# Optimization experiments

Hardware: AMD Instinct MI355X
Metric: run time of the kernel (lower is better)

The kernel has to match this reference:

```python
import jax, jax.numpy as jnp
import numpy as np
import math

NH = 16  # n_head
HS = 64  # head_size = n_embd // n_head


def setup_inputs() -> dict:
    key = jax.random.key(0)
    ks = jax.random.split(key, 7)
    B, T, C, QL, KVL = 2, 2048, 1024, 128, 128
    s = lambda k, shape, fan_in: jax.random.normal(k, shape, jnp.float32) / np.sqrt(fan_in)
    return {
        "x": jax.random.normal(ks[0], (B, T, C), jnp.float32),
        "W_dq": s(ks[1], (QL, C), C),
        "W_uq": s(ks[2], (C, QL), QL),
        "W_dkv": s(ks[3], (KVL, C), C),
        "W_uk": s(ks[4], (C, KVL), KVL),
        "W_uv": s(ks[5], (C, KVL), KVL),
        "W_o": s(ks[6], (C, C), C),
    }


def reference(x, W_dq, W_uq, W_dkv, W_uk, W_uv, W_o):
    B, T, C = x.shape
    kvl = W_dkv.shape[0]
    # absorbed matrices (training branch)
    k_eff = (W_dq.T @ W_uq.T @ W_uk).reshape(NH, HS, kvl)            # (nh, hs, kvl)
    v_eff = (W_uv.T @ W_o.T).reshape(kvl, NH, HS).transpose(1, 0, 2)  # (nh, kvl, hs)
    # latent kv cache
    c_kv = x @ W_dkv.T                                                # (B, T, kvl)
    # query path
    q = (x @ W_dq.T @ W_uq.T).reshape(B, T, NH, HS).transpose(0, 2, 1, 3)  # (B, nh, T, hs)
    # scores: q @ k_eff @ c_kv^T
    ql = jnp.einsum('bhtd,hdl->bhtl', q, k_eff)                       # (B, nh, T, kvl)
    scores = jnp.einsum('bhtl,bsl->bhts', ql, c_kv) / math.sqrt(HS)   # (B, nh, T, T)
    # causal mask
    mask = jnp.tril(jnp.ones((T, T), dtype=bool))
    scores = jnp.where(mask[None, None], scores, -jnp.inf)
    attn = jax.nn.softmax(scores, axis=-1)
    # output: attn @ c_kv @ v_eff
    ctx = jnp.einsum('bhts,bsl->bhtl', attn, c_kv)                    # (B, nh, T, kvl)
    y = jnp.einsum('bhtl,hld->bhtd', ctx, v_eff)                      # (B, nh, T, hs)
    y = y.transpose(0, 2, 1, 3).reshape(B, T, C)
    return y, c_kv
```

## Files before the change

### kernel.cpp

```cpp
#include <hip/hip_runtime.h>
#include <hip/hip_bf16.h>

typedef __hip_bfloat16 bf16;
typedef __attribute__((ext_vector_type(8))) short short8;
typedef __attribute__((ext_vector_type(4))) float f32x4;

#define NHD 16
#define HSD 64
#define KVLD 128
#define QLD 128
#define CD 1024
#define BD 2
#define TD 2048

__device__ __forceinline__ short8 ld8(const bf16* p) { return *(const short8*)p; }
__device__ __forceinline__ void st8(bf16* p, short8 v) { *(short8*)p = v; }

__device__ __forceinline__ void st4(bf16* p, float4 a) {
    union { short4 s; bf16 h[4]; } u;
    u.h[0] = __float2bfloat16(a.x); u.h[1] = __float2bfloat16(a.y);
    u.h[2] = __float2bfloat16(a.z); u.h[3] = __float2bfloat16(a.w);
    *(short4*)p = u.s;
}
__device__ __forceinline__ void st4f(bf16* p, f32x4 a) {
    union { short4 s; bf16 h[4]; } u;
    u.h[0] = __float2bfloat16(a[0]); u.h[1] = __float2bfloat16(a[1]);
    u.h[2] = __float2bfloat16(a[2]); u.h[3] = __float2bfloat16(a[3]);
    *(short4*)p = u.s;
}

__global__ __launch_bounds__(256) void k_pre(const float* __restrict__ wuq,
                                             const float* __restrict__ wuk,
                                             const float* __restrict__ wdq,
                                             const float* __restrict__ wdkv,
                                             const float* __restrict__ wuv,
                                             const float* __restrict__ wo,
                                             float* __restrict__ m1p,
                                             float* __restrict__ G,
                                             bf16* __restrict__ wqkv_bf,
                                             bf16* __restrict__ veffT_bf) {
    __shared__ __align__(16) char arena[49152];
    const int b = blockIdx.x;
    const int tid = threadIdx.x;
    if (b < 128) {
        const int part = b >> 4, ig = b & 15;
        const int i = ig * 8 + (tid >> 5);
        const int j4 = (tid & 31) << 2;
        const float* wq = wuq + (size_t)part * 128 * QLD;
        const float* wk = wuk + (size_t)part * 128 * KVLD;
        float4 acc = make_float4(0.f, 0.f, 0.f, 0.f);
        for (int c0 = 0; c0 < 128; c0 += 8) {
            float a[8]; float4 kv[8];
#pragma unroll
            for (int u = 0; u < 8; ++u) {
                a[u] = wq[(c0 + u) * QLD + i];
                kv[u] = *(const float4*)(wk + (c0 + u) * KVLD + j4);
            }
#pragma unroll
            for (int u = 0; u < 8; ++u) {
                acc.x = fmaf(a[u], kv[u].x, acc.x);
                acc.y = fmaf(a[u], kv[u].y, acc.y);
                acc.z = fmaf(a[u], kv[u].z, acc.z);
                acc.w = fmaf(a[u], kv[u].w, acc.w);
            }
        }
        *(float4*)(m1p + (size_t)part * 16384 + (size_t)i * 128 + j4) = acc;
    } else if (b < 256) {
        const int b1 = b - 128;
        const int h = b1 >> 3, p8 = b1 & 7;
        const int p = p8 * 16 + (tid >> 4);
        const int i8 = (tid & 15) << 3;
        float acc[8];
#pragma unroll
        for (int t = 0; t < 8; ++t) acc[t] = 0.f;
        const float* wdqp = wdq + (size_t)p * CD + h * 64;
        const float* wuqh = wuq + (size_t)(h * 64) * QLD + i8;
        for (int d0 = 0; d0 < 64; d0 += 8) {
            float a[8]; float4 b0[8], b1v[8];
#pragma unroll
            for (int u = 0; u < 8; ++u) {
                a[u] = wdqp[d0 + u];
                b0[u] = *(const float4*)(wuqh + (d0 + u) * QLD);
                b1v[u] = *(const float4*)(wuqh + (d0 + u) * QLD + 4);
            }
#pragma unroll
            for (int u = 0; u < 8; ++u) {
                acc[0] = fmaf(a[u], b0[u].x, acc[0]);  acc[1] = fmaf(a[u], b0[u].y, acc[1]);
                acc[2] = fmaf(a[u], b0[u].z, acc[2]);  acc[3] = fmaf(a[u], b0[u].w, acc[3]);
                acc[4] = fmaf(a[u], b1v[u].x, acc[4]); acc[5] = fmaf(a[u], b1v[u].y, acc[5]);
                acc[6] = fmaf(a[u], b1v[u].z, acc[6]); acc[7] = fmaf(a[u], b1v[u].w, acc[7]);
            }
        }
        float* dst = G + (size_t)h * 16384 + (size_t)p * 128 + i8;
        *(float4*)dst = make_float4(acc[0], acc[1], acc[2], acc[3]);
        *(float4*)(dst + 4) = make_float4(acc[4], acc[5], acc[6], acc[7]);
    } else if (b < 320) {
        const int r = (b - 256) * 4 + (tid >> 6);
        const int lane = tid & 63;
        const float* src = (r < 128) ? (wdq + (size_t)r * CD) : (wdkv + (size_t)(r - 128) * CD);
        float4 f[4];
#pragma unroll
        for (int k = 0; k < 4; ++k) f[k] = ((const float4*)src)[lane + k * 64];
#pragma unroll
        for (int k = 0; k < 4; ++k)
            st4(wqkv_bf + (size_t)r * CD + (lane + k * 64) * 4, f[k]);
    } else {
        const int b3 = b - 320;
        const int cc0 = b3 * 4;
        float* woS = (float*)arena;
        float* wuvS = (float*)arena + 4096;
#pragma unroll
        for (int k = 0; k < 4; ++k)
            ((float4*)woS)[tid + k * 256] = ((const float4*)(wo + (size_t)cc0 * CD))[tid + k * 256];

        const int r = tid >> 6;
        const int lh = tid & 63;
        float4 pf[8];
#pragma unroll
        for (int t = 0; t < 8; ++t)
            pf[t] = ((const float4*)wuv)[t * 256 + tid];

        float a0 = 0.f, a1 = 0.f;
        for (int ch = 0; ch < 16; ++ch) {
            __syncthreads();
#pragma unroll
            for (int t = 0; t < 8; ++t)
                ((float4*)wuvS)[t * 256 + tid] = pf[t];
            __syncthreads();
            if (ch < 15) {
#pragma unroll
                for (int t = 0; t < 8; ++t)
                    pf[t] = ((const float4*)wuv)[(ch + 1) * 2048 + t * 256 + tid];
            }
            const float* wr = woS + r * 1024 + ch * 64;
            const float2* vv = (const float2*)wuvS + lh;
            for (int cb = 0; cb < 64; cb += 8) {
                float wv[8]; float2 v[8];
#pragma unroll
                for (int u = 0; u < 8; ++u) {
                    wv[u] = wr[cb + u];
                    v[u] = vv[(cb + u) * 64];
                }
#pragma unroll
                for (int u = 0; u < 8; ++u) {
                    a0 = fmaf(wv[u], v[u].x, a0);
                    a1 = fmaf(wv[u], v[u].y, a1);
                }
            }
        }
        union { short2 s; bf16 h2[2]; } u;
        u.h2[0] = __float2bfloat16(a0);
        u.h2[1] = __float2bfloat16(a1);
        *(short2*)(veffT_bf + (size_t)(cc0 + r) * KVLD + lh * 2) = u.s;
    }
}

__global__ __launch_bounds__(256) void k_main(const float* __restrict__ x,
                                              const bf16* __restrict__ wqkv_bf,
                                              const float* __restrict__ m1p,
                                              const float* __restrict__ G,
                                              bf16* __restrict__ q1_bf,
                                              float* __restrict__ ckv_out,
                                              bf16* __restrict__ ckv_bf,
                                              bf16* __restrict__ ckvT_bf,
                                              bf16* __restrict__ Et_bf) {
    __shared__ __align__(16) char arena[39168];
    const int blk = blockIdx.x;
    const int tid = threadIdx.x;

    if (blk < 256) {
        const int m0 = blk * 16;
        const int w = tid >> 6, lane = tid & 63, m16 = lane & 15, g = lane >> 4;
        bf16* As = (bf16*)arena;
        bf16* Bs = (bf16*)(arena + 2304);

        const int arow = tid >> 4, akc = (tid & 15) << 2;
        const float* axp = x + (size_t)(m0 + arow) * CD + akc;
        int brow[8], bkc[8];
#pragma unroll
        for (int kk = 0; kk < 8; ++kk) {
            int v = tid + kk * 256;
            brow[kk] = v >> 3; bkc[kk] = (v & 7) << 3;
        }

        float4 pA = *(const float4*)(axp);
        short8 pB[8];
#pragma unroll
        for (int kk = 0; kk < 8; ++kk)
            pB[kk] = ld8(wqkv_bf + (size_t)brow[kk] * CD + bkc[kk]);

        f32x4 acc[4];
#pragma unroll
        for (int nb = 0; nb < 4; ++nb) acc[nb] = (f32x4){0.f, 0.f, 0.f, 0.f};

        for (int k0 = 0; k0 < CD; k0 += 64) {
            __syncthreads();
            st4(As + arow * 72 + akc, pA);
#pragma unroll
            for (int kk = 0; kk < 8; ++kk)
                st8(Bs + brow[kk] * 72 + bkc[kk], pB[kk]);
            __syncthreads();
            if (k0 + 64 < CD) {
                pA = *(const float4*)(axp + k0 + 64);
#pragma unroll
                for (int kk = 0; kk < 8; ++kk)
                    pB[kk] = ld8(wqkv_bf + (size_t)brow[kk] * CD + k0 + 64 + bkc[kk]);
            }
            short8 aF[2];
#pragma unroll
            for (int kf = 0; kf < 2; ++kf)
                aF[kf] = ld8(As + m16 * 72 + kf * 32 + g * 8);
#pragma unroll
            for (int nb = 0; nb < 4; ++nb)
#pragma unroll
                for (int kf = 0; kf < 2; ++kf) {
                    short8 bF = ld8(Bs + (w * 64 + nb * 16 + m16) * 72 + kf * 32 + g * 8);
                    acc[nb] = __builtin_amdgcn_mfma_f32_16x16x32_bf16(aF[kf], bF, acc[nb], 0, 0, 0);
                }
        }

        const int bb = m0 >> 11;
        const int tl0 = (m0 & 2047) + g * 4;
#pragma unroll
        for (int nb = 0; nb < 4; ++nb) {
            int col = w * 64 + nb * 16 + m16;
            if (col < 128) {
#pragma unroll
                for (int r = 0; r < 4; ++r)
                    q1_bf[(size_t)(m0 + g * 4 + r) * QLD + col] = __float2bfloat16(acc[nb][r]);
            } else {
                int l = col - 128;
                union { short4 s; bf16 h[4]; } pk;
#pragma unroll
                for (int r = 0; r < 4; ++r) {
                    int t = m0 + g * 4 + r;
                    float v = acc[nb][r];
                    ckv_out[(size_t)t * KVLD + l] = v;
                    bf16 hv = __float2bfloat16(v);
                    ckv_bf[(size_t)t * KVLD + l] = hv;
                    pk.h[r] = hv;
                }
                *(short4*)(ckvT_bf + ((size_t)bb * KVLD + l) * TD + tl0) = pk.s;
            }
        }
    } else {
        const int b2 = blk - 256;
        const int h = b2 >> 4, lb = b2 & 15;
        float* m1s = (float*)arena;
        for (int v = tid; v < 1024; v += 256) {
            int p = v >> 3, lq = v & 7;
            float t0[8];
#pragma unroll
            for (int part = 0; part < 8; ++part)
                t0[part] = m1p[(size_t)part * 16384 + (size_t)p * 128 + lb * 8 + lq];
            float s0 = 0.f;
#pragma unroll
            for (int part = 0; part < 8; ++part) s0 += t0[part];
            m1s[v] = s0;
        }
        __syncthreads();
        const int lq = tid >> 5, i4 = (tid & 31) << 2;
        const float* Gh = G + (size_t)h * 16384;
        float4 acc = make_float4(0.f, 0.f, 0.f, 0.f);
        for (int p0 = 0; p0 < 128; p0 += 8) {
            float4 g[8]; float a[8];
#pragma unroll
            for (int u = 0; u < 8; ++u) {
                g[u] = *(const float4*)(Gh + (p0 + u) * 128 + i4);
                a[u] = m1s[(p0 + u) * 8 + lq];
            }
#pragma unroll
            for (int u = 0; u < 8; ++u) {
                acc.x = fmaf(a[u], g[u].x, acc.x);
                acc.y = fmaf(a[u], g[u].y, acc.y);
                acc.z = fmaf(a[u], g[u].z, acc.z);
                acc.w = fmaf(a[u], g[u].w, acc.w);
            }
        }
        const float sc = 0.1803368801f;
        const int l = lb * 8 + lq;
        st4(Et_bf + ((size_t)h * 128 + l) * 128 + i4,
            make_float4(sc * acc.x, sc * acc.y, sc * acc.z, sc * acc.w));
    }
}

__global__ __launch_bounds__(512, 4) void k_flash(const bf16* __restrict__ Q1_bf,
                                                  const bf16* __restrict__ Et_bf,
                                                  const bf16* __restrict__ ckv_bf,
                                                  const bf16* __restrict__ ckvT_bf,
                                                  const bf16* __restrict__ veffT_bf,
                                                  float* __restrict__ yout) {
    const int h = blockIdx.x & 15;
    const int b = blockIdx.x >> 4;
    const int qlo = blockIdx.y;
    const int qhi = 31 - qlo;
    const int tid = threadIdx.x;
    const int w = tid >> 6;
    const int ws = w >> 2;
    const int wq = w & 3;
    const int lane = tid & 63;
    const int m16 = lane & 15;
    const int g = lane >> 4;
    const int myqt = ws ? qlo : qhi;
    const int row0 = myqt * 64;

    __shared__ __align__(16) short smem_raw[27136];
    bf16* smem = (bf16*)smem_raw;
    bf16* kvN = smem;
    bf16* kvT = smem + 8704;
    bf16* pS  = smem + 17920 + w * 1152;
    bf16* bufLo = kvT;
    bf16* vT = smem + 17920;

    {
        const bf16* q1hi = Q1_bf + ((size_t)(b * TD + qhi * 64)) * QLD;
        const bf16* q1lo = Q1_bf + ((size_t)(b * TD + qlo * 64)) * QLD;
#pragma unroll
        for (int k = 0; k < 2; ++k) {
            int v = tid + k * 512;
            int row = v >> 4, cv = (v & 15) << 3;
            st8(kvN + row * 136 + cv, ld8(q1hi + row * QLD + cv));
            st8(bufLo + row * 136 + cv, ld8(q1lo + row * QLD + cv));
        }
    }
    __syncthreads();
    bf16* myQ1 = ws ? bufLo : kvN;
    {
        short8 aq[4];
#pragma unroll
        for (int kf = 0; kf < 4; ++kf)
            aq[kf] = ld8(myQ1 + (wq * 16 + m16) * 136 + kf * 32 + g * 8);
        const bf16* Eh = Et_bf + (size_t)h * QLD * KVLD;
        f32x4 qc[8];
#pragma unroll
        for (int nb = 0; nb < 8; ++nb) qc[nb] = (f32x4){0.f, 0.f, 0.f, 0.f};
#pragma unroll
        for (int nb = 0; nb < 8; ++nb)
#pragma unroll
            for (int kf = 0; kf < 4; ++kf) {
                short8 bq = ld8(Eh + (nb * 16 + m16) * QLD + kf * 32 + g * 8);
                qc[nb] = __builtin_amdgcn_mfma_f32_16x16x32_bf16(bq, aq[kf], qc[nb], 0, 0, 0);
            }
        __syncthreads();
#pragma unroll
        for (int nb = 0; nb < 8; ++nb)
            st4f(myQ1 + (wq * 16 + m16) * 136 + nb * 16 + g * 4, qc[nb]);
    }
    __syncthreads();
    short8 qlA[4];
#pragma unroll
    for (int kf = 0; kf < 4; ++kf)
        qlA[kf] = ld8(myQ1 + (wq * 16 + m16) * 136 + kf * 32 + g * 8);

    f32x4 cx[8];
#pragma unroll
    for (int nb = 0; nb < 8; ++nb) cx[nb] = (f32x4){0.f, 0.f, 0.f, 0.f};
    float den = 0.f;
    float mrow = -INFINITY;
    const int rg = row0 + wq * 16 + m16;

    const bf16* ckb = ckv_bf + (size_t)b * TD * KVLD;
    const bf16* ckTb = ckvT_bf + (size_t)b * KVLD * TD;

    int nrow[2], ncol[2], trow[2], tcol[2];
#pragma unroll
    for (int k = 0; k < 2; ++k) {
        int v = tid + k * 512;
        nrow[k] = v >> 4; ncol[k] = (v & 15) << 3;
        trow[k] = v >> 3; tcol[k] = (v & 7) << 3;
    }
    short8 pfN[2], pfT[2];
#pragma unroll
    for (int k = 0; k < 2; ++k) {
        pfN[k] = ld8(ckb + (size_t)nrow[k] * KVLD + ncol[k]);
        pfT[k] = ld8(ckTb + (size_t)trow[k] * TD + tcol[k]);
    }

    for (int tile = 0; tile <= qhi; ++tile) {
        const int s0 = tile * 64;
        __syncthreads();
#pragma unroll
        for (int k = 0; k < 2; ++k) {
            st8(kvN + nrow[k] * 136 + ncol[k], pfN[k]);
            st8(kvT + trow[k] * 72 + tcol[k], pfT[k]);
        }
        __syncthreads();
        if (tile < qhi) {
            const int s1 = s0 + 64;
#pragma unroll
            for (int k = 0; k < 2; ++k) {
                pfN[k] = ld8(ckb + (size_t)(s1 + nrow[k]) * KVLD + ncol[k]);
                pfT[k] = ld8(ckTb + (size_t)trow[k] * TD + s1 + tcol[k]);
            }
        }

        if (ws == 0 || tile <= qlo) {
            f32x4 sa[4];
#pragma unroll
            for (int nb = 0; nb < 4; ++nb) sa[nb] = (f32x4){0.f, 0.f, 0.f, 0.f};
            __builtin_amdgcn_s_setprio(1);
#pragma unroll
            for (int nb = 0; nb < 4; ++nb)
#pragma unroll
                for (int kf = 0; kf < 4; ++kf) {
                    short8 ak = ld8(kvN + (nb * 16 + m16) * 136 + kf * 32 + g * 8);
                    sa[nb] = __builtin_amdgcn_mfma_f32_16x16x32_bf16(ak, qlA[kf], sa[nb], 0, 0, 0);
                }
            __builtin_amdgcn_s_setprio(0);

            if (tile == myqt) {
#pragma unroll
                for (int nb = 0; nb < 4; ++nb)
#pragma unroll
                    for (int r = 0; r < 4; ++r) {
                        int sg = s0 + nb * 16 + g * 4 + r;
                        if (sg > rg) sa[nb][r] = -INFINITY;
                    }
            }

            float mloc = sa[0][0];
#pragma unroll
            for (int nb = 0; nb < 4; ++nb)
#pragma unroll
                for (int r = 0; r < 4; ++r) mloc = fmaxf(mloc, sa[nb][r]);
            mloc = fmaxf(mloc, __shfl_xor(mloc, 16));
            mloc = fmaxf(mloc, __shfl_xor(mloc, 32));
            if (__any(mloc > mrow + 8.f)) {
                float mt = fmaxf(mrow, mloc);
                float al = exp2f(mrow - mt);
                mrow = mt;
                den *= al;
#pragma unroll
                for (int nb = 0; nb < 8; ++nb)
#pragma unroll
                    for (int r = 0; r < 4; ++r) cx[nb][r] *= al;
            }

            float psum = 0.f;
#pragma unroll
            for (int nb = 0; nb < 4; ++nb) {
                float4 p4;
                p4.x = exp2f(sa[nb][0] - mrow);
                p4.y = exp2f(sa[nb][1] - mrow);
                p4.z = exp2f(sa[nb][2] - mrow);
                p4.w = exp2f(sa[nb][3] - mrow);
                psum += (p4.x + p4.y) + (p4.z + p4.w);
                st4(pS + m16 * 72 + nb * 16 + g * 4, p4);
            }
            psum += __shfl_xor(psum, 16);
            psum += __shfl_xor(psum, 32);
            den += psum;
            __builtin_amdgcn_wave_barrier();

            short8 pA[2];
#pragma unroll
            for (int kf = 0; kf < 2; ++kf)
                pA[kf] = ld8(pS + m16 * 72 + kf * 32 + g * 8);
            __builtin_amdgcn_s_setprio(1);
#pragma unroll
            for (int nb = 0; nb < 8; ++nb)
#pragma unroll
                for (int kf = 0; kf < 2; ++kf) {
                    short8 av = ld8(kvT + (nb * 16 + m16) * 72 + kf * 32 + g * 8);
                    cx[nb] = __builtin_amdgcn_mfma_f32_16x16x32_bf16(av, pA[kf], cx[nb], 0, 0, 0);
                }
            __builtin_amdgcn_s_setprio(0);
        }
    }

    float invl = 1.f / den;
#pragma unroll
    for (int nb = 0; nb < 8; ++nb)
#pragma unroll
        for (int r = 0; r < 4; ++r) cx[nb][r] *= invl;
    __syncthreads();
    bf16* ctxS = ws ? bufLo : kvN;
#pragma unroll
    for (int nb = 0; nb < 8; ++nb)
        st4f(ctxS + (wq * 16 + m16) * 136 + nb * 16 + g * 4, cx[nb]);
    {
        const bf16* vsrc = veffT_bf + (size_t)h * HSD * KVLD;
#pragma unroll
        for (int k = 0; k < 2; ++k) {
            int v = tid + k * 512;
            int row = v >> 4, cv = (v & 15) << 3;
            st8(vT + row * 136 + cv, ld8(vsrc + row * KVLD + cv));
        }
    }
    __syncthreads();

    short8 cB[4];
#pragma unroll
    for (int kf = 0; kf < 4; ++kf)
        cB[kf] = ld8(ctxS + (wq * 16 + m16) * 136 + kf * 32 + g * 8);
    f32x4 ya[4];
#pragma unroll
    for (int nb = 0; nb < 4; ++nb) ya[nb] = (f32x4){0.f, 0.f, 0.f, 0.f};
#pragma unroll
    for (int nb = 0; nb < 4; ++nb)
#pragma unroll
        for (int kf = 0; kf < 4; ++kf) {
            short8 av = ld8(vT + (nb * 16 + m16) * 136 + kf * 32 + g * 8);
            ya[nb] = __builtin_amdgcn_mfma_f32_16x16x32_bf16(av, cB[kf], ya[nb], 0, 0, 0);
        }
    float* yo = yout + ((size_t)b * TD + rg) * CD + h * HSD;
#pragma unroll
    for (int nb = 0; nb < 4; ++nb)
        *(float4*)(yo + nb * 16 + g * 4) = *(float4*)&ya[nb];
}

extern "C" void kernel_launch(void* const* d_in, const int* in_sizes, int n_in,
                              void* d_out, int out_size, void* d_ws, size_t ws_size,
                              hipStream_t stream) {
    const float* x    = (const float*)d_in[0];
    const float* wdq  = (const float*)d_in[1];
    const float* wuq  = (const float*)d_in[2];
    const float* wdkv = (const float*)d_in[3];
    const float* wuk  = (const float*)d_in[4];
    const float* wuv  = (const float*)d_in[5];
    const float* wo   = (const float*)d_in[6];
    float* yout = (float*)d_out;
    float* ckv_out = yout + (size_t)BD * TD * CD;

    float* ws = (float*)d_ws;
    float* M1P = ws;
    float* G   = M1P + 131072;
    bf16* wqkv_bf  = (bf16*)(G + 262144);
    bf16* Et_bf    = wqkv_bf + 262144;
    bf16* veffT_bf = Et_bf + 262144;
    bf16* ckv_bf   = veffT_bf + 131072;
    bf16* ckvT_bf  = ckv_bf + 524288;
    bf16* Q1_bf    = ckvT_bf + 524288;

    k_pre <<<576, 256, 0, stream>>>(wuq, wuk, wdq, wdkv, wuv, wo,
                                    M1P, G, wqkv_bf, veffT_bf);
    k_main<<<512, 256, 0, stream>>>(x, wqkv_bf, M1P, G,
                                    Q1_bf, ckv_out, ckv_bf, ckvT_bf, Et_bf);

    dim3 grid(32, 16);
    k_flash<<<grid, 512, 0, stream>>>(Q1_bf, Et_bf, ckv_bf, ckvT_bf, veffT_bf, yout);
}
```

Measured before the change: 224.7 us.

## Rebalance flash work to contiguous 128-row tiles and move v_eff build into k_main

The flash kernel stops pairing a low and a high 64-row query tile per block and instead gives each block one contiguous 128-row query tile. The two 4-wave groups share the same KV tiles, and only the last tile is skipped for the first group. The v_eff precompute moves from k_pre to extra blocks of k_main, shortening the k_pre critical path and running alongside the other k_main work. The s_setprio hints around the MFMA loops are removed. Block workloads now vary with the query position, so the causal load balance across blocks becomes uneven, and the launch order with p = 15 - blockIdx.y is meant to start the longest blocks first.

Result: slower. 239.6 us (+6.6%).

```diff
diff --git a/kernel.cpp b/kernel.cpp
--- a/kernel.cpp
+++ b/kernel.cpp
@@ -33,13 +33,9 @@
                                              const float* __restrict__ wuk,
                                              const float* __restrict__ wdq,
                                              const float* __restrict__ wdkv,
-                                             const float* __restrict__ wuv,
-                                             const float* __restrict__ wo,
                                              float* __restrict__ m1p,
                                              float* __restrict__ G,
-                                             bf16* __restrict__ wqkv_bf,
-                                             bf16* __restrict__ veffT_bf) {
-    __shared__ __align__(16) char arena[49152];
+                                             bf16* __restrict__ wqkv_bf) {
     const int b = blockIdx.x;
     const int tid = threadIdx.x;
     if (b < 128) {
@@ -94,7 +90,7 @@
         float* dst = G + (size_t)h * 16384 + (size_t)p * 128 + i8;
         *(float4*)dst = make_float4(acc[0], acc[1], acc[2], acc[3]);
         *(float4*)(dst + 4) = make_float4(acc[4], acc[5], acc[6], acc[7]);
-    } else if (b < 320) {
+    } else {
         const int r = (b - 256) * 4 + (tid >> 6);
         const int lane = tid & 63;
         const float* src = (r < 128) ? (wdq + (size_t)r * CD) : (wdkv + (size_t)(r - 128) * CD);
@@ -104,54 +100,6 @@
 #pragma unroll
         for (int k = 0; k < 4; ++k)
             st4(wqkv_bf + (size_t)r * CD + (lane + k * 64) * 4, f[k]);
-    } else {
-        const int b3 = b - 320;
-        const int cc0 = b3 * 4;
-        float* woS = (float*)arena;
-        float* wuvS = (float*)arena + 4096;
-#pragma unroll
-        for (int k = 0; k < 4; ++k)
-            ((float4*)woS)[tid + k * 256] = ((const float4*)(wo + (size_t)cc0 * CD))[tid + k * 256];
-
-        const int r = tid >> 6;
-        const int lh = tid & 63;
-        float4 pf[8];
-#pragma unroll
-        for (int t = 0; t < 8; ++t)
-            pf[t] = ((const float4*)wuv)[t * 256 + tid];
-
-        float a0 = 0.f, a1 = 0.f;
-        for (int ch = 0; ch < 16; ++ch) {
-            __syncthreads();
-#pragma unroll
-            for (int t = 0; t < 8; ++t)
-                ((float4*)wuvS)[t * 256 + tid] = pf[t];
-            __syncthreads();
-            if (ch < 15) {
-#pragma unroll
-                for (int t = 0; t < 8; ++t)
-                    pf[t] = ((const float4*)wuv)[(ch + 1) * 2048 + t * 256 + tid];
-            }
-            const float* wr = woS + r * 1024 + ch * 64;
-            const float2* vv = (const float2*)wuvS + lh;
-            for (int cb = 0; cb < 64; cb += 8) {
-                float wv[8]; float2 v[8];
-#pragma unroll
-                for (int u = 0; u < 8; ++u) {
-                    wv[u] = wr[cb + u];
-                    v[u] = vv[(cb + u) * 64];
-                }
-#pragma unroll
-                for (int u = 0; u < 8; ++u) {
-                    a0 = fmaf(wv[u], v[u].x, a0);
-                    a1 = fmaf(wv[u], v[u].y, a1);
-                }
-            }
-        }
-        union { short2 s; bf16 h2[2]; } u;
-        u.h2[0] = __float2bfloat16(a0);
-        u.h2[1] = __float2bfloat16(a1);
-        *(short2*)(veffT_bf + (size_t)(cc0 + r) * KVLD + lh * 2) = u.s;
     }
 }
 
@@ -159,12 +107,15 @@
                                               const bf16* __restrict__ wqkv_bf,
                                               const float* __restrict__ m1p,
                                               const float* __restrict__ G,
+                                              const float* __restrict__ wuv,
+                                              const float* __restrict__ wo,
                                               bf16* __restrict__ q1_bf,
                                               float* __restrict__ ckv_out,
                                               bf16* __restrict__ ckv_bf,
                                               bf16* __restrict__ ckvT_bf,
-                                              bf16* __restrict__ Et_bf) {
-    __shared__ __align__(16) char arena[39168];
+                                              bf16* __restrict__ Et_bf,
+                                              bf16* __restrict__ veffT_bf) {
+    __shared__ __align__(16) char arena[49152];
     const int blk = blockIdx.x;
     const int tid = threadIdx.x;
 
@@ -243,7 +194,7 @@
                 *(short4*)(ckvT_bf + ((size_t)bb * KVLD + l) * TD + tl0) = pk.s;
             }
         }
-    } else {
+    } else if (blk < 512) {
         const int b2 = blk - 256;
         const int h = b2 >> 4, lb = b2 & 15;
         float* m1s = (float*)arena;
@@ -281,6 +232,54 @@
         const int l = lb * 8 + lq;
         st4(Et_bf + ((size_t)h * 128 + l) * 128 + i4,
             make_float4(sc * acc.x, sc * acc.y, sc * acc.z, sc * acc.w));
+    } else {
+        const int b3 = blk - 512;
+        const int cc0 = b3 * 4;
+        float* woS = (float*)arena;
+        float* wuvS = (float*)arena + 4096;
+#pragma unroll
+        for (int k = 0; k < 4; ++k)
+            ((float4*)woS)[tid + k * 256] = ((const float4*)(wo + (size_t)cc0 * CD))[tid + k * 256];
+
+        const int r = tid >> 6;
+        const int lh = tid & 63;
+        float4 pf[8];
+#pragma unroll
+        for (int t = 0; t < 8; ++t)
+            pf[t] = ((const float4*)wuv)[t * 256 + tid];
+
+        float a0 = 0.f, a1 = 0.f;
+        for (int ch = 0; ch < 16; ++ch) {
+            __syncthreads();
+#pragma unroll
+            for (int t = 0; t < 8; ++t)
+                ((float4*)wuvS)[t * 256 + tid] = pf[t];
+            __syncthreads();
+            if (ch < 15) {
+#pragma unroll
+                for (int t = 0; t < 8; ++t)
+                    pf[t] = ((const float4*)wuv)[(ch + 1) * 2048 + t * 256 + tid];
+            }
+            const float* wr = woS + r * 1024 + ch * 64;
+            const float2* vv = (const float2*)wuvS + lh;
+            for (int cb = 0; cb < 64; cb += 8) {
+                float wv[8]; float2 v[8];
+#pragma unroll
+                for (int u = 0; u < 8; ++u) {
+                    wv[u] = wr[cb + u];
+                    v[u] = vv[(cb + u) * 64];
+                }
+#pragma unroll
+                for (int u = 0; u < 8; ++u) {
+                    a0 = fmaf(wv[u], v[u].x, a0);
+                    a1 = fmaf(wv[u], v[u].y, a1);
+                }
+            }
+        }
+        union { short2 s; bf16 h2[2]; } u;
+        u.h2[0] = __float2bfloat16(a0);
+        u.h2[1] = __float2bfloat16(a1);
+        *(short2*)(veffT_bf + (size_t)(cc0 + r) * KVLD + lh * 2) = u.s;
     }
 }
 
@@ -292,17 +291,16 @@
                                                   float* __restrict__ yout) {
     const int h = blockIdx.x & 15;
     const int b = blockIdx.x >> 4;
-    const int qlo = blockIdx.y;
-    const int qhi = 31 - qlo;
+    const int p = 15 - blockIdx.y;
     const int tid = threadIdx.x;
     const int w = tid >> 6;
     const int ws = w >> 2;
-    const int wq = w & 3;
+    const int wql = w & 3;
     const int lane = tid & 63;
     const int m16 = lane & 15;
     const int g = lane >> 4;
-    const int myqt = ws ? qlo : qhi;
-    const int row0 = myqt * 64;
+    const int row0 = p * 128;
+    const int nlast = 2 * p + 1;
 
     __shared__ __align__(16) short smem_raw[27136];
     bf16* smem = (bf16*)smem_raw;
@@ -313,14 +311,14 @@
     bf16* vT = smem + 17920;
 
     {
-        const bf16* q1hi = Q1_bf + ((size_t)(b * TD + qhi * 64)) * QLD;
-        const bf16* q1lo = Q1_bf + ((size_t)(b * TD + qlo * 64)) * QLD;
+        const bf16* q1a = Q1_bf + ((size_t)(b * TD + row0)) * QLD;
+        const bf16* q1b = Q1_bf + ((size_t)(b * TD + row0 + 64)) * QLD;
 #pragma unroll
         for (int k = 0; k < 2; ++k) {
             int v = tid + k * 512;
             int row = v >> 4, cv = (v & 15) << 3;
-            st8(kvN + row * 136 + cv, ld8(q1hi + row * QLD + cv));
-            st8(bufLo + row * 136 + cv, ld8(q1lo + row * QLD + cv));
+            st8(kvN + row * 136 + cv, ld8(q1a + row * QLD + cv));
+            st8(bufLo + row * 136 + cv, ld8(q1b + row * QLD + cv));
         }
     }
     __syncthreads();
@@ -329,7 +327,7 @@
         short8 aq[4];
 #pragma unroll
         for (int kf = 0; kf < 4; ++kf)
-            aq[kf] = ld8(myQ1 + (wq * 16 + m16) * 136 + kf * 32 + g * 8);
+            aq[kf] = ld8(myQ1 + (wql * 16 + m16) * 136 + kf * 32 + g * 8);
         const bf16* Eh = Et_bf + (size_t)h * QLD * KVLD;
         f32x4 qc[8];
 #pragma unroll
@@ -344,20 +342,21 @@
         __syncthreads();
 #pragma unroll
         for (int nb = 0; nb < 8; ++nb)
-            st4f(myQ1 + (wq * 16 + m16) * 136 + nb * 16 + g * 4, qc[nb]);
+            st4f(myQ1 + (wql * 16 + m16) * 136 + nb * 16 + g * 4, qc[nb]);
     }
     __syncthreads();
     short8 qlA[4];
 #pragma unroll
     for (int kf = 0; kf < 4; ++kf)
-        qlA[kf] = ld8(myQ1 + (wq * 16 + m16) * 136 + kf * 32 + g * 8);
+        qlA[kf] = ld8(myQ1 + (wql * 16 + m16) * 136 + kf * 32 + g * 8);
 
     f32x4 cx[8];
 #pragma unroll
     for (int nb = 0; nb < 8; ++nb) cx[nb] = (f32x4){0.f, 0.f, 0.f, 0.f};
     float den = 0.f;
     float mrow = -INFINITY;
-    const int rg = row0 + wq * 16 + m16;
+    const int rg = row0 + w * 16 + m16;
+    const int maskTile = 2 * p + ws;
 
     const bf16* ckb = ckv_bf + (size_t)b * TD * KVLD;
     const bf16* ckTb = ckvT_bf + (size_t)b * KVLD * TD;
@@ -376,7 +375,7 @@
         pfT[k] = ld8(ckTb + (size_t)trow[k] * TD + tcol[k]);
     }
 
-    for (int tile = 0; tile <= qhi; ++tile) {
+    for (int tile = 0; tile <= nlast; ++tile) {
         const int s0 = tile * 64;
         __syncthreads();
 #pragma unroll
@@ -385,7 +384,7 @@
             st8(kvT + trow[k] * 72 + tcol[k], pfT[k]);
         }
         __syncthreads();
-        if (tile < qhi) {
+        if (tile < nlast) {
             const int s1 = s0 + 64;
 #pragma unroll
             for (int k = 0; k < 2; ++k) {
@@ -394,11 +393,10 @@
             }
         }
 
-        if (ws == 0 || tile <= qlo) {
+        if (ws == 1 || tile < nlast) {
             f32x4 sa[4];
 #pragma unroll
             for (int nb = 0; nb < 4; ++nb) sa[nb] = (f32x4){0.f, 0.f, 0.f, 0.f};
-            __builtin_amdgcn_s_setprio(1);
 #pragma unroll
             for (int nb = 0; nb < 4; ++nb)
 #pragma unroll
@@ -406,9 +404,8 @@
                     short8 ak = ld8(kvN + (nb * 16 + m16) * 136 + kf * 32 + g * 8);
                     sa[nb] = __builtin_amdgcn_mfma_f32_16x16x32_bf16(ak, qlA[kf], sa[nb], 0, 0, 0);
                 }
-            __builtin_amdgcn_s_setprio(0);
-
-            if (tile == myqt) {
+
+            if (tile == maskTile) {
 #pragma unroll
                 for (int nb = 0; nb < 4; ++nb)
 #pragma unroll
@@ -456,7 +453,6 @@
 #pragma unroll
             for (int kf = 0; kf < 2; ++kf)
                 pA[kf] = ld8(pS + m16 * 72 + kf * 32 + g * 8);
-            __builtin_amdgcn_s_setprio(1);
 #pragma unroll
             for (int nb = 0; nb < 8; ++nb)
 #pragma unroll
@@ -464,7 +460,6 @@
                     short8 av = ld8(kvT + (nb * 16 + m16) * 72 + kf * 32 + g * 8);
                     cx[nb] = __builtin_amdgcn_mfma_f32_16x16x32_bf16(av, pA[kf], cx[nb], 0, 0, 0);
                 }
-            __builtin_amdgcn_s_setprio(0);
         }
     }
 
@@ -477,7 +472,7 @@
     bf16* ctxS = ws ? bufLo : kvN;
 #pragma unroll
     for (int nb = 0; nb < 8; ++nb)
-        st4f(ctxS + (wq * 16 + m16) * 136 + nb * 16 + g * 4, cx[nb]);
+        st4f(ctxS + (wql * 16 + m16) * 136 + nb * 16 + g * 4, cx[nb]);
     {
         const bf16* vsrc = veffT_bf + (size_t)h * HSD * KVLD;
 #pragma unroll
@@ -492,7 +487,7 @@
     short8 cB[4];
 #pragma unroll
     for (int kf = 0; kf < 4; ++kf)
-        cB[kf] = ld8(ctxS + (wq * 16 + m16) * 136 + kf * 32 + g * 8);
+        cB[kf] = ld8(ctxS + (wql * 16 + m16) * 136 + kf * 32 + g * 8);
     f32x4 ya[4];
 #pragma unroll
     for (int nb = 0; nb < 4; ++nb) ya[nb] = (f32x4){0.f, 0.f, 0.f, 0.f};
@@ -532,10 +527,9 @@
     bf16* ckvT_bf  = ckv_bf + 524288;
     bf16* Q1_bf    = ckvT_bf + 524288;
 
-    k_pre <<<576, 256, 0, stream>>>(wuq, wuk, wdq, wdkv, wuv, wo,
-                                    M1P, G, wqkv_bf, veffT_bf);
-    k_main<<<512, 256, 0, stream>>>(x, wqkv_bf, M1P, G,
-                                    Q1_bf, ckv_out, ckv_bf, ckvT_bf, Et_bf);
+    k_pre <<<320, 256, 0, stream>>>(wuq, wuk, wdq, wdkv, M1P, G, wqkv_bf);
+    k_main<<<768, 256, 0, stream>>>(x, wqkv_bf, M1P, G, wuv, wo,
+                                    Q1_bf, ckv_out, ckv_bf, ckvT_bf, Et_bf, veffT_bf);
 
     dim3 grid(32, 16);
     k_flash<<<grid, 512, 0, stream>>>(Q1_bf, Et_bf, ckv_bf, ckvT_bf, veffT_bf, yout);
```
